# Kernel optimization log

Measured on AMD Instinct MI355X. Metric: run time of the kernel, lower is better.

The kernel has to match this reference:

```python
import jax, jax.numpy as jnp
import numpy as np

EMBED_DIM = 1024
NUM_HEADS = 16
HEAD_DIM = EMBED_DIM // NUM_HEADS  # 64
B, NQ, NK = 4, 1024, 2048


def setup_inputs() -> dict:
    key = jax.random.key(0)
    ks = jax.random.split(key, 13)
    s = 1.0 / np.sqrt(EMBED_DIM)
    inp = {
        "query": jax.random.normal(ks[0], (B, NQ, EMBED_DIM), jnp.float32),
        "key": jax.random.normal(ks[1], (B, NK, EMBED_DIM), jnp.float32),
        "value": jax.random.normal(ks[2], (B, NK, EMBED_DIM), jnp.float32),
        # positive multiplicity weights per key element
        "key_multiplicities": jax.random.uniform(ks[3], (B, NK), jnp.float32, 0.1, 4.0),
        "wq_w": jax.random.normal(ks[4], (EMBED_DIM, EMBED_DIM), jnp.float32) * s,
        "wq_b": jnp.zeros((EMBED_DIM,), jnp.float32),
        "wk_w": jax.random.normal(ks[5], (EMBED_DIM, EMBED_DIM), jnp.float32) * s,
        "wk_b": jnp.zeros((EMBED_DIM,), jnp.float32),
        "wv_w": jax.random.normal(ks[6], (EMBED_DIM, EMBED_DIM), jnp.float32) * s,
        "wv_b": jnp.zeros((EMBED_DIM,), jnp.float32),
        "wo_w": jax.random.normal(ks[7], (EMBED_DIM, EMBED_DIM), jnp.float32) * s,
        "wo_b": jnp.zeros((EMBED_DIM,), jnp.float32),
    }
    return inp


def _split_heads(x, b, n):
    # (b, n, h*d) -> (b, h, n, d)
    return x.reshape(b, n, NUM_HEADS, HEAD_DIM).transpose(0, 2, 1, 3)


def reference(query, key, value, key_multiplicities,
              wq_w, wq_b, wk_w, wk_b, wv_w, wv_b, wo_w, wo_b):
    b, n_q, _ = query.shape
    _, n_k, _ = key.shape
    q = _split_heads(query @ wq_w.T + wq_b, b, n_q)   # (b, h, n_q, d)
    k = _split_heads(key @ wk_w.T + wk_b, b, n_k)     # (b, h, n_k, d)
    v = _split_heads(value @ wv_w.T + wv_b, b, n_k)   # (b, h, n_k, d)
    scale = 1.0 / jnp.sqrt(jnp.asarray(HEAD_DIM, q.dtype))
    scores = jnp.einsum("bhqd,bhkd->bhqk", q, k) * scale
    # multiplicities weight each key: softmax_i(m_i * exp(s_i)) == softmax(s_i + log m_i)
    logits = scores + jnp.log(key_multiplicities)[:, None, None, :]
    attn = jax.nn.softmax(logits, axis=-1)            # (b, h, n_q, n_k)
    out = jnp.einsum("bhqk,bhkd->bhqd", attn, v)
    out = out.transpose(0, 2, 1, 3).reshape(b, n_q, NUM_HEADS * HEAD_DIM)
    return out @ wo_w.T + wo_b
```

## Files before the change

kernel.cpp:

```cpp
#include <hip/hip_runtime.h>
#include <hip/hip_bf16.h>
#include <stdint.h>
#include <stddef.h>

typedef __attribute__((ext_vector_type(8))) short bf16x8;
typedef __attribute__((ext_vector_type(4))) short short4v;
typedef __attribute__((ext_vector_type(4))) float f32x4;
typedef __attribute__((ext_vector_type(2))) uint32_t u32x2;
typedef __attribute__((ext_vector_type(4))) uint32_t u32x4;

#define MFMA16(a, b, c) __builtin_amdgcn_mfma_f32_16x16x32_bf16((a), (b), (c), 0, 0, 0)

__device__ __forceinline__ short f2bf(float f) {
    uint32_t u = __builtin_bit_cast(uint32_t, f);
    u = (u + 0x7FFFu + ((u >> 16) & 1u)) >> 16;
    return (short)(uint16_t)u;
}

__device__ __forceinline__ uint32_t pkbf(float a, float b) {
#if __has_builtin(__builtin_amdgcn_cvt_pk_bf16_f32)
    auto r = __builtin_amdgcn_cvt_pk_bf16_f32(a, b);
    return __builtin_bit_cast(uint32_t, r);
#else
    return (uint32_t)(uint16_t)f2bf(a) | ((uint32_t)(uint16_t)f2bf(b) << 16);
#endif
}

__device__ __forceinline__ float fexp2(float x) {
#if __has_builtin(__builtin_amdgcn_exp2f)
    return __builtin_amdgcn_exp2f(x);
#else
    return exp2f(x);
#endif
}

__device__ __forceinline__ void gload16(const short* g, short* l) {
    __builtin_amdgcn_global_load_lds(
        (const __attribute__((address_space(1))) unsigned int*)g,
        (__attribute__((address_space(3))) unsigned int*)l, 16, 0, 0);
}

__global__ __launch_bounds__(256) void prep_kernel(
        const float* __restrict__ w0, const float* __restrict__ w1,
        const float* __restrict__ w2, const float* __restrict__ w3,
        const float* __restrict__ q, const float* __restrict__ k,
        const float* __restrict__ v, const float* __restrict__ m,
        short* __restrict__ wb, short* __restrict__ Qa,
        short* __restrict__ Ka, short* __restrict__ Va,
        float* __restrict__ lm) {
    const int z = blockIdx.z, bx = blockIdx.x;
    if (z == 7) {
        if (bx >= 4) return;
        const int i = (bx * 256 + threadIdx.x) * 8;
        f32x4 a = *(const f32x4*)(m + i);
        f32x4 b = *(const f32x4*)(m + i + 4);
        f32x4 oa, ob;
        #pragma unroll
        for (int j = 0; j < 4; ++j) { oa[j] = __log2f(a[j]); ob[j] = __log2f(b[j]); }
        *(f32x4*)(lm + i) = oa;
        *(f32x4*)(lm + i + 4) = ob;
        return;
    }
    const float* src;
    short* dst;
    int nb;
    if (z < 4) {
        src = (z == 0) ? w0 : (z == 1) ? w1 : (z == 2) ? w2 : w3;
        dst = wb + (size_t)z * 1048576;
        nb = 512;
    } else if (z == 4) { src = q; dst = Qa; nb = 2048; }
    else if (z == 5)   { src = k; dst = Ka; nb = 4096; }
    else               { src = v; dst = Va; nb = 4096; }
    if (bx >= nb) return;
    const size_t i = ((size_t)bx * 256 + threadIdx.x) * 8;
    f32x4 a = *(const f32x4*)(src + i);
    f32x4 b = *(const f32x4*)(src + i + 4);
    u32x4 o = { pkbf(a[0], a[1]), pkbf(a[2], a[3]), pkbf(b[0], b[1]), pkbf(b[2], b[3]) };
    *(u32x4*)(dst + i) = o;
}


__global__ __launch_bounds__(256) void gemm_qk_kernel(
        const short* __restrict__ Qa, const short* __restrict__ Ka,
        const short* __restrict__ wb, const float* __restrict__ wq_b,
        const float* __restrict__ wk_b, short* __restrict__ Qp,
        short* __restrict__ Kp) {
    __shared__ short As[128 * 32];
    __shared__ short Bs[128 * 32];

    const int y = blockIdx.y;
    const short* A; const short* W; const float* bias; short* out; int nshift, tm;
    if (y < 32) { A = Qa; W = wb;           bias = wq_b; out = Qp; nshift = 10; tm = y * 128; }
    else        { A = Ka; W = wb + 1048576; bias = wk_b; out = Kp; nshift = 11; tm = (y - 32) * 128; }

    const int t = threadIdx.x, lane = t & 63, w = t >> 6;
    const int wr = w >> 1, wc = w & 1;
    const int qd = lane >> 4, c = lane & 15;
    const int tn = blockIdx.x * 128;

    f32x4 acc[4][4];
    #pragma unroll
    for (int i = 0; i < 4; ++i)
        #pragma unroll
        for (int j = 0; j < 4; ++j) acc[i][j] = (f32x4){0.f, 0.f, 0.f, 0.f};

    const int r0 = w * 16 + (lane >> 2);
    const int qc = (lane & 3) ^ ((lane >> 3) & 3);
    const short* ga0 = A + (size_t)(tm + r0) * 1024 + qc * 8;
    const short* ga1 = ga0 + 64 * 1024;
    const short* gb0 = W + (size_t)(tn + r0) * 1024 + qc * 8;
    const short* gb1 = gb0 + 64 * 1024;
    short* la0 = &As[w * 512];
    short* la1 = &As[w * 512 + 2048];
    short* lb0 = &Bs[w * 512];
    short* lb1 = &Bs[w * 512 + 2048];
    const int swz = (qd ^ ((c >> 1) & 3)) * 8;

    for (int k0 = 0; k0 < 1024; k0 += 32) {
        __syncthreads();
        gload16(ga0 + k0, la0);
        gload16(ga1 + k0, la1);
        gload16(gb0 + k0, lb0);
        gload16(gb1 + k0, lb1);
        __syncthreads();
        bf16x8 af[4], bfr[4];
        #pragma unroll
        for (int rt = 0; rt < 4; ++rt)
            af[rt] = *(const bf16x8*)&As[(wr * 64 + rt * 16 + c) * 32 + swz];
        #pragma unroll
        for (int ct = 0; ct < 4; ++ct)
            bfr[ct] = *(const bf16x8*)&Bs[(wc * 64 + ct * 16 + c) * 32 + swz];
        #pragma unroll
        for (int rt = 0; rt < 4; ++rt)
            #pragma unroll
            for (int ct = 0; ct < 4; ++ct)
                acc[rt][ct] = MFMA16(af[rt], bfr[ct], acc[rt][ct]);
    }

    float bv[4];
    #pragma unroll
    for (int ct = 0; ct < 4; ++ct) bv[ct] = bias[tn + wc * 64 + ct * 16 + c];

    const int mask = (1 << nshift) - 1;
    #pragma unroll
    for (int rt = 0; rt < 4; ++rt)
        #pragma unroll
        for (int ct = 0; ct < 4; ++ct) {
            const int cg = tn + wc * 64 + ct * 16 + c;
            const int h = cg >> 6, d = cg & 63;
            #pragma unroll
            for (int r = 0; r < 4; ++r) {
                const int rg = tm + wr * 64 + rt * 16 + qd * 4 + r;
                const int bb = rg >> nshift, n = rg & mask;
                out[((((size_t)(bb * 16 + h)) << nshift) + n) * 64 + d] =
                    f2bf(acc[rt][ct][r] + bv[ct]);
            }
        }
}

__global__ __launch_bounds__(256) void gemm_v_kernel(
        const short* __restrict__ Va, const short* __restrict__ W,
        const float* __restrict__ bias, short* __restrict__ Vt) {
    __shared__ short As[128 * 32];
    __shared__ short Bs[128 * 32];

    const int t = threadIdx.x, lane = t & 63, w = t >> 6;
    const int wr = w >> 1, wc = w & 1;
    const int qd = lane >> 4, c = lane & 15;
    const int tm = blockIdx.y * 128, tn = blockIdx.x * 128;

    f32x4 acc[4][4];
    #pragma unroll
    for (int i = 0; i < 4; ++i)
        #pragma unroll
        for (int j = 0; j < 4; ++j) acc[i][j] = (f32x4){0.f, 0.f, 0.f, 0.f};

    const int r0 = w * 16 + (lane >> 2);
    const int qc = (lane & 3) ^ ((lane >> 3) & 3);
    const short* ga0 = Va + (size_t)(tm + r0) * 1024 + qc * 8;
    const short* ga1 = ga0 + 64 * 1024;
    const short* gb0 = W + (size_t)(tn + r0) * 1024 + qc * 8;
    const short* gb1 = gb0 + 64 * 1024;
    short* la0 = &As[w * 512];
    short* la1 = &As[w * 512 + 2048];
    short* lb0 = &Bs[w * 512];
    short* lb1 = &Bs[w * 512 + 2048];
    const int swz = (qd ^ ((c >> 1) & 3)) * 8;

    for (int k0 = 0; k0 < 1024; k0 += 32) {
        __syncthreads();
        gload16(ga0 + k0, la0);
        gload16(ga1 + k0, la1);
        gload16(gb0 + k0, lb0);
        gload16(gb1 + k0, lb1);
        __syncthreads();
        bf16x8 af[4], bfr[4];
        #pragma unroll
        for (int rt = 0; rt < 4; ++rt)
            af[rt] = *(const bf16x8*)&As[(wr * 64 + rt * 16 + c) * 32 + swz];
        #pragma unroll
        for (int ct = 0; ct < 4; ++ct)
            bfr[ct] = *(const bf16x8*)&Bs[(wc * 64 + ct * 16 + c) * 32 + swz];
        #pragma unroll
        for (int rt = 0; rt < 4; ++rt)
            #pragma unroll
            for (int ct = 0; ct < 4; ++ct)
                acc[rt][ct] = MFMA16(af[rt], bfr[ct], acc[rt][ct]);
    }

    float bv[4];
    #pragma unroll
    for (int ct = 0; ct < 4; ++ct) bv[ct] = bias[tn + wc * 64 + ct * 16 + c];

    #pragma unroll
    for (int rt = 0; rt < 4; ++rt)
        #pragma unroll
        for (int ct = 0; ct < 4; ++ct) {
            const int cg = tn + wc * 64 + ct * 16 + c;
            const int h = cg >> 6, d = cg & 63;
            const int rg0 = tm + wr * 64 + rt * 16 + qd * 4;
            const int bb = rg0 >> 11, n = rg0 & 2047;
            u32x2 pk = { pkbf(acc[rt][ct][0] + bv[ct], acc[rt][ct][1] + bv[ct]),
                         pkbf(acc[rt][ct][2] + bv[ct], acc[rt][ct][3] + bv[ct]) };
            *(u32x2*)&Vt[((((size_t)(bb * 16 + h)) * 64 + d) << 11) + n] = pk;
        }
}

__global__ __launch_bounds__(256) void gemm_o_kernel(
        const short* __restrict__ Ob, const short* __restrict__ W,
        const float* __restrict__ bias, float* __restrict__ out) {
    __shared__ short As[128 * 32];
    __shared__ short Bs[64 * 32];

    const int t = threadIdx.x, lane = t & 63, w = t >> 6;
    const int wr = w >> 1, wc = w & 1;
    const int qd = lane >> 4, c = lane & 15;
    const int tm = blockIdx.y * 128, tn = blockIdx.x * 64;

    f32x4 acc[4][2];
    #pragma unroll
    for (int i = 0; i < 4; ++i)
        #pragma unroll
        for (int j = 0; j < 2; ++j) acc[i][j] = (f32x4){0.f, 0.f, 0.f, 0.f};

    const int r0 = w * 16 + (lane >> 2);
    const int qc = (lane & 3) ^ ((lane >> 3) & 3);
    const short* ga0 = Ob + (size_t)(tm + r0) * 1024 + qc * 8;
    const short* ga1 = ga0 + 64 * 1024;
    const short* gb0 = W + (size_t)(tn + r0) * 1024 + qc * 8;
    short* la0 = &As[w * 512];
    short* la1 = &As[w * 512 + 2048];
    short* lb0 = &Bs[w * 512];
    const int swz = (qd ^ ((c >> 1) & 3)) * 8;

    for (int k0 = 0; k0 < 1024; k0 += 32) {
        __syncthreads();
        gload16(ga0 + k0, la0);
        gload16(ga1 + k0, la1);
        gload16(gb0 + k0, lb0);
        __syncthreads();
        bf16x8 af[4], bfr[2];
        #pragma unroll
        for (int rt = 0; rt < 4; ++rt)
            af[rt] = *(const bf16x8*)&As[(wr * 64 + rt * 16 + c) * 32 + swz];
        #pragma unroll
        for (int ct = 0; ct < 2; ++ct)
            bfr[ct] = *(const bf16x8*)&Bs[(wc * 32 + ct * 16 + c) * 32 + swz];
        #pragma unroll
        for (int rt = 0; rt < 4; ++rt)
            #pragma unroll
            for (int ct = 0; ct < 2; ++ct)
                acc[rt][ct] = MFMA16(af[rt], bfr[ct], acc[rt][ct]);
    }

    float bv[2];
    #pragma unroll
    for (int ct = 0; ct < 2; ++ct) bv[ct] = bias[tn + wc * 32 + ct * 16 + c];

    #pragma unroll
    for (int rt = 0; rt < 4; ++rt)
        #pragma unroll
        for (int ct = 0; ct < 2; ++ct) {
            const int cg = tn + wc * 32 + ct * 16 + c;
            #pragma unroll
            for (int r = 0; r < 4; ++r) {
                const int rg = tm + wr * 64 + rt * 16 + qd * 4 + r;
                out[(size_t)rg * 1024 + cg] = acc[rt][ct][r] + bv[ct];
            }
        }
}

__global__ __launch_bounds__(256, 2) void attn_kernel(
        const short* __restrict__ Qp, const short* __restrict__ Kp,
        const short* __restrict__ Vt, const float* __restrict__ logm,
        short* __restrict__ Ob) {
    __shared__ short UKP[128 * 136];
    __shared__ short Vs[64 * 136];
    __shared__ float Lm[128];
    short* Ks = UKP;
    short* Ps = UKP;

    const int qt = blockIdx.x, bh = blockIdx.y;
    const int b = bh >> 4;
    const int t = threadIdx.x, lane = t & 63, w = t >> 6;
    const int qd = lane >> 4, c = lane & 15;
    const float SC = 0.18033688011112042f;

    bf16x8 qf[2][2];
    #pragma unroll
    for (int ct = 0; ct < 2; ++ct)
        #pragma unroll
        for (int kd = 0; kd < 2; ++kd)
            qf[ct][kd] = *(const bf16x8*)(Qp +
                ((size_t)bh * 1024 + qt * 128 + w * 32 + ct * 16 + c) * 64 + kd * 32 + qd * 8);

    float mo[2] = {-1e30f, -1e30f};
    float li[2] = {0.f, 0.f};
    f32x4 oacc[2][4];
    #pragma unroll
    for (int i = 0; i < 2; ++i)
        #pragma unroll
        for (int j = 0; j < 4; ++j) oacc[i][j] = (f32x4){0.f, 0.f, 0.f, 0.f};

    const short* kg = Kp + ((size_t)bh * 2048 + (t >> 1)) * 64 + (t & 1) * 32;
    const short* vg = Vt + ((size_t)bh * 64 + (t >> 2)) * 2048 + (t & 3) * 32;

    for (int kt = 0; kt < 16; ++kt) {
        const short* kp = kg + (size_t)kt * 128 * 64;
        bf16x8 kx0 = *(const bf16x8*)(kp);
        bf16x8 kx1 = *(const bf16x8*)(kp + 8);
        bf16x8 kx2 = *(const bf16x8*)(kp + 16);
        bf16x8 kx3 = *(const bf16x8*)(kp + 24);
        const short* vp = vg + kt * 128;
        bf16x8 vx0 = *(const bf16x8*)(vp);
        bf16x8 vx1 = *(const bf16x8*)(vp + 8);
        bf16x8 vx2 = *(const bf16x8*)(vp + 16);
        bf16x8 vx3 = *(const bf16x8*)(vp + 24);
        float lmv = 0.f;
        if (t < 128) lmv = logm[b * 2048 + kt * 128 + t];

        {
            const int kr = t >> 1, kc = (t & 1) * 32;
            *(bf16x8*)&Ks[kr * 72 + kc]      = kx0;
            *(bf16x8*)&Ks[kr * 72 + kc + 8]  = kx1;
            *(bf16x8*)&Ks[kr * 72 + kc + 16] = kx2;
            *(bf16x8*)&Ks[kr * 72 + kc + 24] = kx3;
            const int vr = t >> 2, vc = (t & 3) * 32;
            *(bf16x8*)&Vs[vr * 136 + vc]      = vx0;
            *(bf16x8*)&Vs[vr * 136 + vc + 8]  = vx1;
            *(bf16x8*)&Vs[vr * 136 + vc + 16] = vx2;
            *(bf16x8*)&Vs[vr * 136 + vc + 24] = vx3;
            if (t < 128) Lm[t] = lmv;
        }
        __syncthreads();

        f32x4 s[8][2];
        #pragma unroll
        for (int rt = 0; rt < 8; ++rt) {
            bf16x8 a0 = *(const bf16x8*)&Ks[(rt * 16 + c) * 72 + qd * 8];
            bf16x8 a1 = *(const bf16x8*)&Ks[(rt * 16 + c) * 72 + 32 + qd * 8];
            #pragma unroll
            for (int ct = 0; ct < 2; ++ct) {
                f32x4 z = (f32x4){0.f, 0.f, 0.f, 0.f};
                f32x4 p0 = MFMA16(a0, qf[ct][0], z);
                s[rt][ct] = MFMA16(a1, qf[ct][1], p0);
            }
        }
        __syncthreads();

        float mt[2] = {-1e30f, -1e30f};
        #pragma unroll
        for (int rt = 0; rt < 8; ++rt) {
            f32x4 lv = *(const f32x4*)&Lm[rt * 16 + qd * 4];
            #pragma unroll
            for (int ct = 0; ct < 2; ++ct)
                #pragma unroll
                for (int r = 0; r < 4; ++r) {
                    float vv = s[rt][ct][r] * SC + lv[r];
                    s[rt][ct][r] = vv;
                    mt[ct] = fmaxf(mt[ct], vv);
                }
        }
        float al[2], snew[2];
        #pragma unroll
        for (int ct = 0; ct < 2; ++ct) {
            mt[ct] = fmaxf(mt[ct], __shfl_xor(mt[ct], 16));
            mt[ct] = fmaxf(mt[ct], __shfl_xor(mt[ct], 32));
            float mn = fmaxf(mo[ct], mt[ct]);
            al[ct] = fexp2(mo[ct] - mn);
            mo[ct] = mn;
            snew[ct] = 0.f;
        }
        #pragma unroll
        for (int rt = 0; rt < 8; ++rt) {
            #pragma unroll
            for (int ct = 0; ct < 2; ++ct) {
                float p0 = fexp2(s[rt][ct][0] - mo[ct]);
                float p1 = fexp2(s[rt][ct][1] - mo[ct]);
                float p2 = fexp2(s[rt][ct][2] - mo[ct]);
                float p3 = fexp2(s[rt][ct][3] - mo[ct]);
                snew[ct] += (p0 + p1) + (p2 + p3);
                u32x2 pk = { pkbf(p0, p1), pkbf(p2, p3) };
                *(u32x2*)&Ps[(w * 32 + ct * 16 + c) * 136 + rt * 16 + qd * 4] = pk;
            }
        }
        #pragma unroll
        for (int ct = 0; ct < 2; ++ct) {
            snew[ct] += __shfl_xor(snew[ct], 16);
            snew[ct] += __shfl_xor(snew[ct], 32);
            li[ct] = li[ct] * al[ct] + snew[ct];
        }

        float alr[2][4];
        #pragma unroll
        for (int rtq = 0; rtq < 2; ++rtq)
            #pragma unroll
            for (int r = 0; r < 4; ++r)
                alr[rtq][r] = __shfl(al[rtq], qd * 4 + r);
        #pragma unroll
        for (int rtq = 0; rtq < 2; ++rtq)
            #pragma unroll
            for (int ct = 0; ct < 4; ++ct)
                #pragma unroll
                for (int r = 0; r < 4; ++r)
                    oacc[rtq][ct][r] *= alr[rtq][r];

        #pragma unroll
        for (int kk = 0; kk < 4; ++kk) {
            bf16x8 pf[2], vf[4];
            #pragma unroll
            for (int rtq = 0; rtq < 2; ++rtq)
                pf[rtq] = *(const bf16x8*)&Ps[(w * 32 + rtq * 16 + c) * 136 + kk * 32 + qd * 8];
            #pragma unroll
            for (int ct = 0; ct < 4; ++ct)
                vf[ct] = *(const bf16x8*)&Vs[(ct * 16 + c) * 136 + kk * 32 + qd * 8];
            #pragma unroll
            for (int rtq = 0; rtq < 2; ++rtq)
                #pragma unroll
                for (int ct = 0; ct < 4; ++ct)
                    oacc[rtq][ct] = MFMA16(pf[rtq], vf[ct], oacc[rtq][ct]);
        }
        __syncthreads();
    }

    const int h = bh & 15;
    float inv[2][4];
    #pragma unroll
    for (int rtq = 0; rtq < 2; ++rtq)
        #pragma unroll
        for (int r = 0; r < 4; ++r)
            inv[rtq][r] = 1.f / __shfl(li[rtq], qd * 4 + r);
    #pragma unroll
    for (int rtq = 0; rtq < 2; ++rtq)
        #pragma unroll
        for (int ct = 0; ct < 4; ++ct)
            #pragma unroll
            for (int r = 0; r < 4; ++r) {
                const int qg = qt * 128 + w * 32 + rtq * 16 + qd * 4 + r;
                const int e = h * 64 + ct * 16 + c;
                Ob[((size_t)(b * 1024 + qg)) * 1024 + e] = f2bf(oacc[rtq][ct][r] * inv[rtq][r]);
            }
}

extern "C" void kernel_launch(void* const* d_in, const int* in_sizes, int n_in,
                              void* d_out, int out_size, void* d_ws, size_t ws_size,
                              hipStream_t stream) {
    (void)in_sizes; (void)n_in; (void)out_size; (void)ws_size;
    const float* query = (const float*)d_in[0];
    const float* key   = (const float*)d_in[1];
    const float* value = (const float*)d_in[2];
    const float* mult  = (const float*)d_in[3];
    const float* wq_w  = (const float*)d_in[4];
    const float* wq_b  = (const float*)d_in[5];
    const float* wk_w  = (const float*)d_in[6];
    const float* wk_b  = (const float*)d_in[7];
    const float* wv_w  = (const float*)d_in[8];
    const float* wv_b  = (const float*)d_in[9];
    const float* wo_w  = (const float*)d_in[10];
    const float* wo_b  = (const float*)d_in[11];
    float* out = (float*)d_out;

    char* ws = (char*)d_ws;
    const size_t MB = 1024 * 1024;
    short* wb = (short*)(ws + 0 * MB);
    short* Qa = (short*)(ws + 8 * MB);
    short* Ka = (short*)(ws + 16 * MB);
    short* Va = (short*)(ws + 32 * MB);
    short* Vt = (short*)(ws + 8 * MB);
    short* Ob = (short*)(ws + 32 * MB);
    short* Qp = (short*)(ws + 48 * MB);
    short* Kp = (short*)(ws + 56 * MB);
    float* lm = (float*)(ws + 72 * MB);

    prep_kernel<<<dim3(4096, 1, 8), 256, 0, stream>>>(
        wq_w, wk_w, wv_w, wo_w, query, key, value, mult, wb, Qa, Ka, Va, lm);
    gemm_qk_kernel<<<dim3(8, 96), 256, 0, stream>>>(Qa, Ka, wb, wq_b, wk_b, Qp, Kp);
    gemm_v_kernel<<<dim3(8, 64), 256, 0, stream>>>(Va, wb + 2097152, wv_b, Vt);
    attn_kernel<<<dim3(8, 64), 256, 0, stream>>>(Qp, Kp, Vt, lm, Ob);
    gemm_o_kernel<<<dim3(16, 32), 256, 0, stream>>>(Ob, wb + 3145728, wo_b, out);
}
```

Before: 297.4 us.

## Merge Q/K/V projections into one launch and halve attention query tile

```diff
diff --git a/kernel.cpp b/kernel.cpp
--- a/kernel.cpp
+++ b/kernel.cpp
@@ -79,19 +79,20 @@
     *(u32x4*)(dst + i) = o;
 }
 
-
-__global__ __launch_bounds__(256) void gemm_qk_kernel(
+__global__ __launch_bounds__(256) void proj_kernel(
         const short* __restrict__ Qa, const short* __restrict__ Ka,
-        const short* __restrict__ wb, const float* __restrict__ wq_b,
-        const float* __restrict__ wk_b, short* __restrict__ Qp,
-        short* __restrict__ Kp) {
+        const short* __restrict__ Va, const short* __restrict__ wb,
+        const float* __restrict__ wq_b, const float* __restrict__ wk_b,
+        const float* __restrict__ wv_b, short* __restrict__ Qp,
+        short* __restrict__ Kp, short* __restrict__ Vt, const int ybase) {
     __shared__ short As[128 * 32];
     __shared__ short Bs[128 * 32];
 
-    const int y = blockIdx.y;
-    const short* A; const short* W; const float* bias; short* out; int nshift, tm;
-    if (y < 32) { A = Qa; W = wb;           bias = wq_b; out = Qp; nshift = 10; tm = y * 128; }
-    else        { A = Ka; W = wb + 1048576; bias = wk_b; out = Kp; nshift = 11; tm = (y - 32) * 128; }
+    const int y = blockIdx.y + ybase;
+    const short* A; const short* W; const float* bias; int mode, tm;
+    if (y < 32)      { A = Qa; W = wb;           bias = wq_b; mode = 0; tm = y * 128; }
+    else if (y < 96) { A = Ka; W = wb + 1048576; bias = wk_b; mode = 1; tm = (y - 32) * 128; }
+    else             { A = Va; W = wb + 2097152; bias = wv_b; mode = 2; tm = (y - 96) * 128; }
 
     const int t = threadIdx.x, lane = t & 63, w = t >> 6;
     const int wr = w >> 1, wc = w & 1;
@@ -141,89 +142,38 @@
     #pragma unroll
     for (int ct = 0; ct < 4; ++ct) bv[ct] = bias[tn + wc * 64 + ct * 16 + c];
 
-    const int mask = (1 << nshift) - 1;
-    #pragma unroll
-    for (int rt = 0; rt < 4; ++rt)
-        #pragma unroll
-        for (int ct = 0; ct < 4; ++ct) {
-            const int cg = tn + wc * 64 + ct * 16 + c;
-            const int h = cg >> 6, d = cg & 63;
-            #pragma unroll
-            for (int r = 0; r < 4; ++r) {
-                const int rg = tm + wr * 64 + rt * 16 + qd * 4 + r;
-                const int bb = rg >> nshift, n = rg & mask;
-                out[((((size_t)(bb * 16 + h)) << nshift) + n) * 64 + d] =
-                    f2bf(acc[rt][ct][r] + bv[ct]);
+    if (mode == 2) {
+        #pragma unroll
+        for (int rt = 0; rt < 4; ++rt)
+            #pragma unroll
+            for (int ct = 0; ct < 4; ++ct) {
+                const int cg = tn + wc * 64 + ct * 16 + c;
+                const int h = cg >> 6, d = cg & 63;
+                const int rg0 = tm + wr * 64 + rt * 16 + qd * 4;
+                const int bb = rg0 >> 11, n = rg0 & 2047;
+                u32x2 pk = { pkbf(acc[rt][ct][0] + bv[ct], acc[rt][ct][1] + bv[ct]),
+                             pkbf(acc[rt][ct][2] + bv[ct], acc[rt][ct][3] + bv[ct]) };
+                *(u32x2*)&Vt[((((size_t)(bb * 16 + h)) * 64 + d) << 11) + n] = pk;
             }
-        }
-}
-
-__global__ __launch_bounds__(256) void gemm_v_kernel(
-        const short* __restrict__ Va, const short* __restrict__ W,
-        const float* __restrict__ bias, short* __restrict__ Vt) {
-    __shared__ short As[128 * 32];
-    __shared__ short Bs[128 * 32];
-
-    const int t = threadIdx.x, lane = t & 63, w = t >> 6;
-    const int wr = w >> 1, wc = w & 1;
-    const int qd = lane >> 4, c = lane & 15;
-    const int tm = blockIdx.y * 128, tn = blockIdx.x * 128;
-
-    f32x4 acc[4][4];
-    #pragma unroll
-    for (int i = 0; i < 4; ++i)
-        #pragma unroll
-        for (int j = 0; j < 4; ++j) acc[i][j] = (f32x4){0.f, 0.f, 0.f, 0.f};
-
-    const int r0 = w * 16 + (lane >> 2);
-    const int qc = (lane & 3) ^ ((lane >> 3) & 3);
-    const short* ga0 = Va + (size_t)(tm + r0) * 1024 + qc * 8;
-    const short* ga1 = ga0 + 64 * 1024;
-    const short* gb0 = W + (size_t)(tn + r0) * 1024 + qc * 8;
-    const short* gb1 = gb0 + 64 * 1024;
-    short* la0 = &As[w * 512];
-    short* la1 = &As[w * 512 + 2048];
-    short* lb0 = &Bs[w * 512];
-    short* lb1 = &Bs[w * 512 + 2048];
-    const int swz = (qd ^ ((c >> 1) & 3)) * 8;
-
-    for (int k0 = 0; k0 < 1024; k0 += 32) {
-        __syncthreads();
-        gload16(ga0 + k0, la0);
-        gload16(ga1 + k0, la1);
-        gload16(gb0 + k0, lb0);
-        gload16(gb1 + k0, lb1);
-        __syncthreads();
-        bf16x8 af[4], bfr[4];
-        #pragma unroll
-        for (int rt = 0; rt < 4; ++rt)
-            af[rt] = *(const bf16x8*)&As[(wr * 64 + rt * 16 + c) * 32 + swz];
-        #pragma unroll
-        for (int ct = 0; ct < 4; ++ct)
-            bfr[ct] = *(const bf16x8*)&Bs[(wc * 64 + ct * 16 + c) * 32 + swz];
-        #pragma unroll
-        for (int rt = 0; rt < 4; ++rt)
-            #pragma unroll
-            for (int ct = 0; ct < 4; ++ct)
-                acc[rt][ct] = MFMA16(af[rt], bfr[ct], acc[rt][ct]);
-    }
-
-    float bv[4];
-    #pragma unroll
-    for (int ct = 0; ct < 4; ++ct) bv[ct] = bias[tn + wc * 64 + ct * 16 + c];
-
-    #pragma unroll
-    for (int rt = 0; rt < 4; ++rt)
-        #pragma unroll
-        for (int ct = 0; ct < 4; ++ct) {
-            const int cg = tn + wc * 64 + ct * 16 + c;
-            const int h = cg >> 6, d = cg & 63;
-            const int rg0 = tm + wr * 64 + rt * 16 + qd * 4;
-            const int bb = rg0 >> 11, n = rg0 & 2047;
-            u32x2 pk = { pkbf(acc[rt][ct][0] + bv[ct], acc[rt][ct][1] + bv[ct]),
-                         pkbf(acc[rt][ct][2] + bv[ct], acc[rt][ct][3] + bv[ct]) };
-            *(u32x2*)&Vt[((((size_t)(bb * 16 + h)) * 64 + d) << 11) + n] = pk;
-        }
+    } else {
+        short* out = (mode == 0) ? Qp : Kp;
+        const int nshift = (mode == 0) ? 10 : 11;
+        const int mask = (1 << nshift) - 1;
+        #pragma unroll
+        for (int rt = 0; rt < 4; ++rt)
+            #pragma unroll
+            for (int ct = 0; ct < 4; ++ct) {
+                const int cg = tn + wc * 64 + ct * 16 + c;
+                const int h = cg >> 6, d = cg & 63;
+                #pragma unroll
+                for (int r = 0; r < 4; ++r) {
+                    const int rg = tm + wr * 64 + rt * 16 + qd * 4 + r;
+                    const int bb = rg >> nshift, n = rg & mask;
+                    out[((((size_t)(bb * 16 + h)) << nshift) + n) * 64 + d] =
+                        f2bf(acc[rt][ct][r] + bv[ct]);
+                }
+            }
+    }
 }
 
 __global__ __launch_bounds__(256) void gemm_o_kernel(
@@ -290,11 +240,11 @@
         }
 }
 
-__global__ __launch_bounds__(256, 2) void attn_kernel(
+__global__ __launch_bounds__(256, 4) void attn_kernel(
         const short* __restrict__ Qp, const short* __restrict__ Kp,
         const short* __restrict__ Vt, const float* __restrict__ logm,
         short* __restrict__ Ob) {
-    __shared__ short UKP[128 * 136];
+    __shared__ short UKP[9216];
     __shared__ short Vs[64 * 136];
     __shared__ float Lm[128];
     short* Ks = UKP;
@@ -306,21 +256,16 @@
     const int qd = lane >> 4, c = lane & 15;
     const float SC = 0.18033688011112042f;
 
-    bf16x8 qf[2][2];
-    #pragma unroll
-    for (int ct = 0; ct < 2; ++ct)
-        #pragma unroll
-        for (int kd = 0; kd < 2; ++kd)
-            qf[ct][kd] = *(const bf16x8*)(Qp +
-                ((size_t)bh * 1024 + qt * 128 + w * 32 + ct * 16 + c) * 64 + kd * 32 + qd * 8);
-
-    float mo[2] = {-1e30f, -1e30f};
-    float li[2] = {0.f, 0.f};
-    f32x4 oacc[2][4];
-    #pragma unroll
-    for (int i = 0; i < 2; ++i)
-        #pragma unroll
-        for (int j = 0; j < 4; ++j) oacc[i][j] = (f32x4){0.f, 0.f, 0.f, 0.f};
+    bf16x8 qf[2];
+    #pragma unroll
+    for (int kd = 0; kd < 2; ++kd)
+        qf[kd] = *(const bf16x8*)(Qp +
+            ((size_t)bh * 1024 + qt * 64 + w * 16 + c) * 64 + kd * 32 + qd * 8);
+
+    float mo = -1e30f, li = 0.f;
+    f32x4 oacc[4];
+    #pragma unroll
+    for (int j = 0; j < 4; ++j) oacc[j] = (f32x4){0.f, 0.f, 0.f, 0.f};
 
     const short* kg = Kp + ((size_t)bh * 2048 + (t >> 1)) * 64 + (t & 1) * 32;
     const short* vg = Vt + ((size_t)bh * 64 + (t >> 2)) * 2048 + (t & 3) * 32;
@@ -354,118 +299,88 @@
         }
         __syncthreads();
 
-        f32x4 s[8][2];
+        f32x4 s[8];
         #pragma unroll
         for (int rt = 0; rt < 8; ++rt) {
             bf16x8 a0 = *(const bf16x8*)&Ks[(rt * 16 + c) * 72 + qd * 8];
             bf16x8 a1 = *(const bf16x8*)&Ks[(rt * 16 + c) * 72 + 32 + qd * 8];
-            #pragma unroll
-            for (int ct = 0; ct < 2; ++ct) {
-                f32x4 z = (f32x4){0.f, 0.f, 0.f, 0.f};
-                f32x4 p0 = MFMA16(a0, qf[ct][0], z);
-                s[rt][ct] = MFMA16(a1, qf[ct][1], p0);
-            }
-        }
-        __syncthreads();
-
-        float mt[2] = {-1e30f, -1e30f};
+            f32x4 z = (f32x4){0.f, 0.f, 0.f, 0.f};
+            s[rt] = MFMA16(a1, qf[1], MFMA16(a0, qf[0], z));
+        }
+        __syncthreads();
+
+        float mt = -1e30f;
         #pragma unroll
         for (int rt = 0; rt < 8; ++rt) {
             f32x4 lv = *(const f32x4*)&Lm[rt * 16 + qd * 4];
             #pragma unroll
-            for (int ct = 0; ct < 2; ++ct)
-                #pragma unroll
-                for (int r = 0; r < 4; ++r) {
-                    float vv = s[rt][ct][r] * SC + lv[r];
-                    s[rt][ct][r] = vv;
-                    mt[ct] = fmaxf(mt[ct], vv);
-                }
-        }
-        float al[2], snew[2];
-        #pragma unroll
-        for (int ct = 0; ct < 2; ++ct) {
-            mt[ct] = fmaxf(mt[ct], __shfl_xor(mt[ct], 16));
-            mt[ct] = fmaxf(mt[ct], __shfl_xor(mt[ct], 32));
-            float mn = fmaxf(mo[ct], mt[ct]);
-            al[ct] = fexp2(mo[ct] - mn);
-            mo[ct] = mn;
-            snew[ct] = 0.f;
-        }
+            for (int r = 0; r < 4; ++r) {
+                float vv = s[rt][r] * SC + lv[r];
+                s[rt][r] = vv;
+                mt = fmaxf(mt, vv);
+            }
+        }
+        mt = fmaxf(mt, __shfl_xor(mt, 16));
+        mt = fmaxf(mt, __shfl_xor(mt, 32));
+        const float mn = fmaxf(mo, mt);
+        const float al = fexp2(mo - mn);
+        mo = mn;
+        float snew = 0.f;
         #pragma unroll
         for (int rt = 0; rt < 8; ++rt) {
-            #pragma unroll
-            for (int ct = 0; ct < 2; ++ct) {
-                float p0 = fexp2(s[rt][ct][0] - mo[ct]);
-                float p1 = fexp2(s[rt][ct][1] - mo[ct]);
-                float p2 = fexp2(s[rt][ct][2] - mo[ct]);
-                float p3 = fexp2(s[rt][ct][3] - mo[ct]);
-                snew[ct] += (p0 + p1) + (p2 + p3);
-                u32x2 pk = { pkbf(p0, p1), pkbf(p2, p3) };
-                *(u32x2*)&Ps[(w * 32 + ct * 16 + c) * 136 + rt * 16 + qd * 4] = pk;
-            }
-        }
-        #pragma unroll
-        for (int ct = 0; ct < 2; ++ct) {
-            snew[ct] += __shfl_xor(snew[ct], 16);
-            snew[ct] += __shfl_xor(snew[ct], 32);
-            li[ct] = li[ct] * al[ct] + snew[ct];
-        }
-
-        float alr[2][4];
-        #pragma unroll
-        for (int rtq = 0; rtq < 2; ++rtq)
+            float p0 = fexp2(s[rt][0] - mo);
+            float p1 = fexp2(s[rt][1] - mo);
+            float p2 = fexp2(s[rt][2] - mo);
+            float p3 = fexp2(s[rt][3] - mo);
+            snew += (p0 + p1) + (p2 + p3);
+            u32x2 pk = { pkbf(p0, p1), pkbf(p2, p3) };
+            *(u32x2*)&Ps[(w * 16 + c) * 136 + rt * 16 + qd * 4] = pk;
+        }
+        snew += __shfl_xor(snew, 16);
+        snew += __shfl_xor(snew, 32);
+        li = li * al + snew;
+
+        float alr[4];
+        #pragma unroll
+        for (int r = 0; r < 4; ++r) alr[r] = __shfl(al, qd * 4 + r);
+        #pragma unroll
+        for (int ct = 0; ct < 4; ++ct)
             #pragma unroll
             for (int r = 0; r < 4; ++r)
-                alr[rtq][r] = __shfl(al[rtq], qd * 4 + r);
-        #pragma unroll
-        for (int rtq = 0; rtq < 2; ++rtq)
-            #pragma unroll
-            for (int ct = 0; ct < 4; ++ct)
-                #pragma unroll
-                for (int r = 0; r < 4; ++r)
-                    oacc[rtq][ct][r] *= alr[rtq][r];
+                oacc[ct][r] *= alr[r];
 
         #pragma unroll
         for (int kk = 0; kk < 4; ++kk) {
-            bf16x8 pf[2], vf[4];
-            #pragma unroll
-            for (int rtq = 0; rtq < 2; ++rtq)
-                pf[rtq] = *(const bf16x8*)&Ps[(w * 32 + rtq * 16 + c) * 136 + kk * 32 + qd * 8];
+            bf16x8 pf = *(const bf16x8*)&Ps[(w * 16 + c) * 136 + kk * 32 + qd * 8];
+            bf16x8 vf[4];
             #pragma unroll
             for (int ct = 0; ct < 4; ++ct)
                 vf[ct] = *(const bf16x8*)&Vs[(ct * 16 + c) * 136 + kk * 32 + qd * 8];
             #pragma unroll
-            for (int rtq = 0; rtq < 2; ++rtq)
-                #pragma unroll
-                for (int ct = 0; ct < 4; ++ct)
-                    oacc[rtq][ct] = MFMA16(pf[rtq], vf[ct], oacc[rtq][ct]);
+            for (int ct = 0; ct < 4; ++ct)
+                oacc[ct] = MFMA16(pf, vf[ct], oacc[ct]);
         }
         __syncthreads();
     }
 
     const int h = bh & 15;
-    float inv[2][4];
-    #pragma unroll
-    for (int rtq = 0; rtq < 2; ++rtq)
-        #pragma unroll
-        for (int r = 0; r < 4; ++r)
-            inv[rtq][r] = 1.f / __shfl(li[rtq], qd * 4 + r);
-    #pragma unroll
-    for (int rtq = 0; rtq < 2; ++rtq)
-        #pragma unroll
-        for (int ct = 0; ct < 4; ++ct)
-            #pragma unroll
-            for (int r = 0; r < 4; ++r) {
-                const int qg = qt * 128 + w * 32 + rtq * 16 + qd * 4 + r;
-                const int e = h * 64 + ct * 16 + c;
-                Ob[((size_t)(b * 1024 + qg)) * 1024 + e] = f2bf(oacc[rtq][ct][r] * inv[rtq][r]);
-            }
+    float inv[4];
+    #pragma unroll
+    for (int r = 0; r < 4; ++r) inv[r] = 1.f / __shfl(li, qd * 4 + r);
+    #pragma unroll
+    for (int ct = 0; ct < 4; ++ct)
+        #pragma unroll
+        for (int r = 0; r < 4; ++r) {
+            const int qg = qt * 64 + w * 16 + qd * 4 + r;
+            const int e = h * 64 + ct * 16 + c;
+            Ob[((size_t)(b * 1024 + qg)) * 1024 + e] = f2bf(oacc[ct][r] * inv[r]);
+        }
 }
 
 extern "C" void kernel_launch(void* const* d_in, const int* in_sizes, int n_in,
                               void* d_out, int out_size, void* d_ws, size_t ws_size,
                               hipStream_t stream) {
-    (void)in_sizes; (void)n_in; (void)out_size; (void)ws_size;
+    (void)in_sizes; (void)n_in; (void)out_size;
     const float* query = (const float*)d_in[0];
     const float* key   = (const float*)d_in[1];
     const float* value = (const float*)d_in[2];
@@ -482,20 +397,36 @@
 
     char* ws = (char*)d_ws;
     const size_t MB = 1024 * 1024;
+    const bool merged = ws_size >= 89 * MB;
+
     short* wb = (short*)(ws + 0 * MB);
     short* Qa = (short*)(ws + 8 * MB);
     short* Ka = (short*)(ws + 16 * MB);
     short* Va = (short*)(ws + 32 * MB);
-    short* Vt = (short*)(ws + 8 * MB);
-    short* Ob = (short*)(ws + 32 * MB);
     short* Qp = (short*)(ws + 48 * MB);
     short* Kp = (short*)(ws + 56 * MB);
-    float* lm = (float*)(ws + 72 * MB);
+    short *Vt, *Ob; float* lm;
+    if (merged) {
+        Vt = (short*)(ws + 72 * MB);
+        Ob = (short*)(ws + 8 * MB);
+        lm = (float*)(ws + 88 * MB);
+    } else {
+        Vt = (short*)(ws + 8 * MB);
+        Ob = (short*)(ws + 32 * MB);
+        lm = (float*)(ws + 72 * MB);
+    }
 
     prep_kernel<<<dim3(4096, 1, 8), 256, 0, stream>>>(
         wq_w, wk_w, wv_w, wo_w, query, key, value, mult, wb, Qa, Ka, Va, lm);
-    gemm_qk_kernel<<<dim3(8, 96), 256, 0, stream>>>(Qa, Ka, wb, wq_b, wk_b, Qp, Kp);
-    gemm_v_kernel<<<dim3(8, 64), 256, 0, stream>>>(Va, wb + 2097152, wv_b, Vt);
-    attn_kernel<<<dim3(8, 64), 256, 0, stream>>>(Qp, Kp, Vt, lm, Ob);
+    if (merged) {
+        proj_kernel<<<dim3(8, 160), 256, 0, stream>>>(
+            Qa, Ka, Va, wb, wq_b, wk_b, wv_b, Qp, Kp, Vt, 0);
+    } else {
+        proj_kernel<<<dim3(8, 96), 256, 0, stream>>>(
+            Qa, Ka, Va, wb, wq_b, wk_b, wv_b, Qp, Kp, Vt, 0);
+        proj_kernel<<<dim3(8, 64), 256, 0, stream>>>(
+            Qa, Ka, Va, wb, wq_b, wk_b, wv_b, Qp, Kp, Vt, 96);
+    }
+    attn_kernel<<<dim3(16, 64), 256, 0, stream>>>(Qp, Kp, Vt, lm, Ob);
     gemm_o_kernel<<<dim3(16, 32), 256, 0, stream>>>(Ob, wb + 3145728, wo_b, out);
 }
```

Result: slower. 318.6 us (+7.1%).

## Merge QKV projections, async-load K/V in attention with XOR swizzle, remap blocks per XCD

Applied to the files above, without the earlier changes.

```diff
diff --git a/kernel.cpp b/kernel.cpp
--- a/kernel.cpp
+++ b/kernel.cpp
@@ -79,19 +79,20 @@
     *(u32x4*)(dst + i) = o;
 }
 
-
-__global__ __launch_bounds__(256) void gemm_qk_kernel(
+__global__ __launch_bounds__(256, 3) void proj_kernel(
         const short* __restrict__ Qa, const short* __restrict__ Ka,
-        const short* __restrict__ wb, const float* __restrict__ wq_b,
-        const float* __restrict__ wk_b, short* __restrict__ Qp,
-        short* __restrict__ Kp) {
+        const short* __restrict__ Va, const short* __restrict__ wb,
+        const float* __restrict__ wq_b, const float* __restrict__ wk_b,
+        const float* __restrict__ wv_b, short* __restrict__ Qp,
+        short* __restrict__ Kp, short* __restrict__ Vt, const int ybase) {
     __shared__ short As[128 * 32];
     __shared__ short Bs[128 * 32];
 
-    const int y = blockIdx.y;
-    const short* A; const short* W; const float* bias; short* out; int nshift, tm;
-    if (y < 32) { A = Qa; W = wb;           bias = wq_b; out = Qp; nshift = 10; tm = y * 128; }
-    else        { A = Ka; W = wb + 1048576; bias = wk_b; out = Kp; nshift = 11; tm = (y - 32) * 128; }
+    const int y = blockIdx.y + ybase;
+    const short* A; const short* W; const float* bias; int mode, tm;
+    if (y < 32)      { A = Qa; W = wb;           bias = wq_b; mode = 0; tm = y * 128; }
+    else if (y < 96) { A = Ka; W = wb + 1048576; bias = wk_b; mode = 1; tm = (y - 32) * 128; }
+    else             { A = Va; W = wb + 2097152; bias = wv_b; mode = 2; tm = (y - 96) * 128; }
 
     const int t = threadIdx.x, lane = t & 63, w = t >> 6;
     const int wr = w >> 1, wc = w & 1;
@@ -141,92 +142,41 @@
     #pragma unroll
     for (int ct = 0; ct < 4; ++ct) bv[ct] = bias[tn + wc * 64 + ct * 16 + c];
 
-    const int mask = (1 << nshift) - 1;
-    #pragma unroll
-    for (int rt = 0; rt < 4; ++rt)
-        #pragma unroll
-        for (int ct = 0; ct < 4; ++ct) {
-            const int cg = tn + wc * 64 + ct * 16 + c;
-            const int h = cg >> 6, d = cg & 63;
-            #pragma unroll
-            for (int r = 0; r < 4; ++r) {
-                const int rg = tm + wr * 64 + rt * 16 + qd * 4 + r;
-                const int bb = rg >> nshift, n = rg & mask;
-                out[((((size_t)(bb * 16 + h)) << nshift) + n) * 64 + d] =
-                    f2bf(acc[rt][ct][r] + bv[ct]);
-            }
-        }
-}
-
-__global__ __launch_bounds__(256) void gemm_v_kernel(
-        const short* __restrict__ Va, const short* __restrict__ W,
-        const float* __restrict__ bias, short* __restrict__ Vt) {
-    __shared__ short As[128 * 32];
-    __shared__ short Bs[128 * 32];
-
-    const int t = threadIdx.x, lane = t & 63, w = t >> 6;
-    const int wr = w >> 1, wc = w & 1;
-    const int qd = lane >> 4, c = lane & 15;
-    const int tm = blockIdx.y * 128, tn = blockIdx.x * 128;
-
-    f32x4 acc[4][4];
-    #pragma unroll
-    for (int i = 0; i < 4; ++i)
-        #pragma unroll
-        for (int j = 0; j < 4; ++j) acc[i][j] = (f32x4){0.f, 0.f, 0.f, 0.f};
-
-    const int r0 = w * 16 + (lane >> 2);
-    const int qc = (lane & 3) ^ ((lane >> 3) & 3);
-    const short* ga0 = Va + (size_t)(tm + r0) * 1024 + qc * 8;
-    const short* ga1 = ga0 + 64 * 1024;
-    const short* gb0 = W + (size_t)(tn + r0) * 1024 + qc * 8;
-    const short* gb1 = gb0 + 64 * 1024;
-    short* la0 = &As[w * 512];
-    short* la1 = &As[w * 512 + 2048];
-    short* lb0 = &Bs[w * 512];
-    short* lb1 = &Bs[w * 512 + 2048];
-    const int swz = (qd ^ ((c >> 1) & 3)) * 8;
-
-    for (int k0 = 0; k0 < 1024; k0 += 32) {
-        __syncthreads();
-        gload16(ga0 + k0, la0);
-        gload16(ga1 + k0, la1);
-        gload16(gb0 + k0, lb0);
-        gload16(gb1 + k0, lb1);
-        __syncthreads();
-        bf16x8 af[4], bfr[4];
-        #pragma unroll
-        for (int rt = 0; rt < 4; ++rt)
-            af[rt] = *(const bf16x8*)&As[(wr * 64 + rt * 16 + c) * 32 + swz];
-        #pragma unroll
-        for (int ct = 0; ct < 4; ++ct)
-            bfr[ct] = *(const bf16x8*)&Bs[(wc * 64 + ct * 16 + c) * 32 + swz];
-        #pragma unroll
-        for (int rt = 0; rt < 4; ++rt)
-            #pragma unroll
-            for (int ct = 0; ct < 4; ++ct)
-                acc[rt][ct] = MFMA16(af[rt], bfr[ct], acc[rt][ct]);
-    }
-
-    float bv[4];
-    #pragma unroll
-    for (int ct = 0; ct < 4; ++ct) bv[ct] = bias[tn + wc * 64 + ct * 16 + c];
-
-    #pragma unroll
-    for (int rt = 0; rt < 4; ++rt)
-        #pragma unroll
-        for (int ct = 0; ct < 4; ++ct) {
-            const int cg = tn + wc * 64 + ct * 16 + c;
-            const int h = cg >> 6, d = cg & 63;
-            const int rg0 = tm + wr * 64 + rt * 16 + qd * 4;
-            const int bb = rg0 >> 11, n = rg0 & 2047;
-            u32x2 pk = { pkbf(acc[rt][ct][0] + bv[ct], acc[rt][ct][1] + bv[ct]),
-                         pkbf(acc[rt][ct][2] + bv[ct], acc[rt][ct][3] + bv[ct]) };
-            *(u32x2*)&Vt[((((size_t)(bb * 16 + h)) * 64 + d) << 11) + n] = pk;
-        }
-}
-
-__global__ __launch_bounds__(256) void gemm_o_kernel(
+    if (mode == 2) {
+        #pragma unroll
+        for (int rt = 0; rt < 4; ++rt)
+            #pragma unroll
+            for (int ct = 0; ct < 4; ++ct) {
+                const int cg = tn + wc * 64 + ct * 16 + c;
+                const int h = cg >> 6, d = cg & 63;
+                const int rg0 = tm + wr * 64 + rt * 16 + qd * 4;
+                const int bb = rg0 >> 11, n = rg0 & 2047;
+                u32x2 pk = { pkbf(acc[rt][ct][0] + bv[ct], acc[rt][ct][1] + bv[ct]),
+                             pkbf(acc[rt][ct][2] + bv[ct], acc[rt][ct][3] + bv[ct]) };
+                *(u32x2*)&Vt[((((size_t)(bb * 16 + h)) * 64 + d) << 11) + n] = pk;
+            }
+    } else {
+        short* out = (mode == 0) ? Qp : Kp;
+        const int nshift = (mode == 0) ? 10 : 11;
+        const int mask = (1 << nshift) - 1;
+        #pragma unroll
+        for (int rt = 0; rt < 4; ++rt)
+            #pragma unroll
+            for (int ct = 0; ct < 4; ++ct) {
+                const int cg = tn + wc * 64 + ct * 16 + c;
+                const int h = cg >> 6, d = cg & 63;
+                #pragma unroll
+                for (int r = 0; r < 4; ++r) {
+                    const int rg = tm + wr * 64 + rt * 16 + qd * 4 + r;
+                    const int bb = rg >> nshift, n = rg & mask;
+                    out[((((size_t)(bb * 16 + h)) << nshift) + n) * 64 + d] =
+                        f2bf(acc[rt][ct][r] + bv[ct]);
+                }
+            }
+    }
+}
+
+__global__ __launch_bounds__(256, 4) void gemm_o_kernel(
         const short* __restrict__ Ob, const short* __restrict__ W,
         const float* __restrict__ bias, float* __restrict__ out) {
     __shared__ short As[128 * 32];
@@ -294,16 +244,18 @@
         const short* __restrict__ Qp, const short* __restrict__ Kp,
         const short* __restrict__ Vt, const float* __restrict__ logm,
         short* __restrict__ Ob) {
-    __shared__ short UKP[128 * 136];
-    __shared__ short Vs[64 * 136];
+    __shared__ short Ps[128 * 128];
+    __shared__ short Vs[64 * 128];
     __shared__ float Lm[128];
-    short* Ks = UKP;
-    short* Ps = UKP;
-
-    const int qt = blockIdx.x, bh = blockIdx.y;
+    short* Ks = Ps;
+
+    const int bid = blockIdx.x;
+    const int xcd = bid & 7, ii = bid >> 3;
+    const int qt = ii >> 3, bh = xcd + ((ii & 7) << 3);
     const int b = bh >> 4;
     const int t = threadIdx.x, lane = t & 63, w = t >> 6;
     const int qd = lane >> 4, c = lane & 15;
+    const int cl = c & 7;
     const float SC = 0.18033688011112042f;
 
     bf16x8 qf[2][2];
@@ -322,48 +274,44 @@
         #pragma unroll
         for (int j = 0; j < 4; ++j) oacc[i][j] = (f32x4){0.f, 0.f, 0.f, 0.f};
 
-    const short* kg = Kp + ((size_t)bh * 2048 + (t >> 1)) * 64 + (t & 1) * 32;
-    const short* vg = Vt + ((size_t)bh * 64 + (t >> 2)) * 2048 + (t & 3) * 32;
+    const short* kgp[4];
+    short* klp[4];
+    const short* vgp[4];
+    short* vlp[4];
+    {
+        const int krow = lane >> 3;
+        const int kchk = (lane & 7) ^ krow;
+        const int vrow = lane >> 4;
+        #pragma unroll
+        for (int i = 0; i < 4; ++i) {
+            const int rk = w * 32 + i * 8 + krow;
+            kgp[i] = Kp + ((size_t)bh * 2048 + rk) * 64 + kchk * 8;
+            klp[i] = &Ks[(w * 4 + i) * 512];
+            const int rv = w * 16 + i * 4 + vrow;
+            const int vchk = (lane & 15) ^ (rv & 7);
+            vgp[i] = Vt + ((size_t)bh * 64 + rv) * 2048 + vchk * 8;
+            vlp[i] = &Vs[(w * 4 + i) * 512];
+        }
+    }
 
     for (int kt = 0; kt < 16; ++kt) {
-        const short* kp = kg + (size_t)kt * 128 * 64;
-        bf16x8 kx0 = *(const bf16x8*)(kp);
-        bf16x8 kx1 = *(const bf16x8*)(kp + 8);
-        bf16x8 kx2 = *(const bf16x8*)(kp + 16);
-        bf16x8 kx3 = *(const bf16x8*)(kp + 24);
-        const short* vp = vg + kt * 128;
-        bf16x8 vx0 = *(const bf16x8*)(vp);
-        bf16x8 vx1 = *(const bf16x8*)(vp + 8);
-        bf16x8 vx2 = *(const bf16x8*)(vp + 16);
-        bf16x8 vx3 = *(const bf16x8*)(vp + 24);
-        float lmv = 0.f;
-        if (t < 128) lmv = logm[b * 2048 + kt * 128 + t];
-
-        {
-            const int kr = t >> 1, kc = (t & 1) * 32;
-            *(bf16x8*)&Ks[kr * 72 + kc]      = kx0;
-            *(bf16x8*)&Ks[kr * 72 + kc + 8]  = kx1;
-            *(bf16x8*)&Ks[kr * 72 + kc + 16] = kx2;
-            *(bf16x8*)&Ks[kr * 72 + kc + 24] = kx3;
-            const int vr = t >> 2, vc = (t & 3) * 32;
-            *(bf16x8*)&Vs[vr * 136 + vc]      = vx0;
-            *(bf16x8*)&Vs[vr * 136 + vc + 8]  = vx1;
-            *(bf16x8*)&Vs[vr * 136 + vc + 16] = vx2;
-            *(bf16x8*)&Vs[vr * 136 + vc + 24] = vx3;
-            if (t < 128) Lm[t] = lmv;
-        }
+        #pragma unroll
+        for (int i = 0; i < 4; ++i) {
+            gload16(kgp[i] + (size_t)kt * 8192, klp[i]);
+            gload16(vgp[i] + kt * 128, vlp[i]);
+        }
+        if (t < 128) Lm[t] = logm[b * 2048 + kt * 128 + t];
         __syncthreads();
 
         f32x4 s[8][2];
         #pragma unroll
         for (int rt = 0; rt < 8; ++rt) {
-            bf16x8 a0 = *(const bf16x8*)&Ks[(rt * 16 + c) * 72 + qd * 8];
-            bf16x8 a1 = *(const bf16x8*)&Ks[(rt * 16 + c) * 72 + 32 + qd * 8];
+            bf16x8 a0 = *(const bf16x8*)&Ks[(rt * 16 + c) * 64 + (qd ^ cl) * 8];
+            bf16x8 a1 = *(const bf16x8*)&Ks[(rt * 16 + c) * 64 + ((4 | qd) ^ cl) * 8];
             #pragma unroll
             for (int ct = 0; ct < 2; ++ct) {
                 f32x4 z = (f32x4){0.f, 0.f, 0.f, 0.f};
-                f32x4 p0 = MFMA16(a0, qf[ct][0], z);
-                s[rt][ct] = MFMA16(a1, qf[ct][1], p0);
+                s[rt][ct] = MFMA16(a1, qf[ct][1], MFMA16(a0, qf[ct][0], z));
             }
         }
         __syncthreads();
@@ -401,7 +349,9 @@
                 float p3 = fexp2(s[rt][ct][3] - mo[ct]);
                 snew[ct] += (p0 + p1) + (p2 + p3);
                 u32x2 pk = { pkbf(p0, p1), pkbf(p2, p3) };
-                *(u32x2*)&Ps[(w * 32 + ct * 16 + c) * 136 + rt * 16 + qd * 4] = pk;
+                const int prow = w * 32 + ct * 16 + c;
+                const int pch = (2 * rt + (qd >> 1)) ^ cl;
+                *(u32x2*)&Ps[prow * 128 + pch * 8 + (qd & 1) * 4] = pk;
             }
         }
         #pragma unroll
@@ -427,13 +377,14 @@
 
         #pragma unroll
         for (int kk = 0; kk < 4; ++kk) {
+            const int lch = ((kk * 4 + qd) ^ cl) * 8;
             bf16x8 pf[2], vf[4];
             #pragma unroll
             for (int rtq = 0; rtq < 2; ++rtq)
-                pf[rtq] = *(const bf16x8*)&Ps[(w * 32 + rtq * 16 + c) * 136 + kk * 32 + qd * 8];
+                pf[rtq] = *(const bf16x8*)&Ps[(w * 32 + rtq * 16 + c) * 128 + lch];
             #pragma unroll
             for (int ct = 0; ct < 4; ++ct)
-                vf[ct] = *(const bf16x8*)&Vs[(ct * 16 + c) * 136 + kk * 32 + qd * 8];
+                vf[ct] = *(const bf16x8*)&Vs[(ct * 16 + c) * 128 + lch];
             #pragma unroll
             for (int rtq = 0; rtq < 2; ++rtq)
                 #pragma unroll
@@ -465,7 +416,7 @@
 extern "C" void kernel_launch(void* const* d_in, const int* in_sizes, int n_in,
                               void* d_out, int out_size, void* d_ws, size_t ws_size,
                               hipStream_t stream) {
-    (void)in_sizes; (void)n_in; (void)out_size; (void)ws_size;
+    (void)in_sizes; (void)n_in; (void)out_size;
     const float* query = (const float*)d_in[0];
     const float* key   = (const float*)d_in[1];
     const float* value = (const float*)d_in[2];
@@ -482,20 +433,36 @@
 
     char* ws = (char*)d_ws;
     const size_t MB = 1024 * 1024;
+    const bool merged = ws_size >= 89 * MB;
+
     short* wb = (short*)(ws + 0 * MB);
     short* Qa = (short*)(ws + 8 * MB);
     short* Ka = (short*)(ws + 16 * MB);
     short* Va = (short*)(ws + 32 * MB);
-    short* Vt = (short*)(ws + 8 * MB);
-    short* Ob = (short*)(ws + 32 * MB);
     short* Qp = (short*)(ws + 48 * MB);
     short* Kp = (short*)(ws + 56 * MB);
-    float* lm = (float*)(ws + 72 * MB);
+    short *Vt, *Ob; float* lm;
+    if (merged) {
+        Vt = (short*)(ws + 72 * MB);
+        Ob = (short*)(ws + 8 * MB);
+        lm = (float*)(ws + 88 * MB);
+    } else {
+        Vt = (short*)(ws + 8 * MB);
+        Ob = (short*)(ws + 32 * MB);
+        lm = (float*)(ws + 72 * MB);
+    }
 
     prep_kernel<<<dim3(4096, 1, 8), 256, 0, stream>>>(
         wq_w, wk_w, wv_w, wo_w, query, key, value, mult, wb, Qa, Ka, Va, lm);
-    gemm_qk_kernel<<<dim3(8, 96), 256, 0, stream>>>(Qa, Ka, wb, wq_b, wk_b, Qp, Kp);
-    gemm_v_kernel<<<dim3(8, 64), 256, 0, stream>>>(Va, wb + 2097152, wv_b, Vt);
-    attn_kernel<<<dim3(8, 64), 256, 0, stream>>>(Qp, Kp, Vt, lm, Ob);
+    if (merged) {
+        proj_kernel<<<dim3(8, 160), 256, 0, stream>>>(
+            Qa, Ka, Va, wb, wq_b, wk_b, wv_b, Qp, Kp, Vt, 0);
+    } else {
+        proj_kernel<<<dim3(8, 96), 256, 0, stream>>>(
+            Qa, Ka, Va, wb, wq_b, wk_b, wv_b, Qp, Kp, Vt, 0);
+        proj_kernel<<<dim3(8, 64), 256, 0, stream>>>(
+            Qa, Ka, Va, wb, wq_b, wk_b, wv_b, Qp, Kp, Vt, 96);
+    }
+    attn_kernel<<<dim3(512), 256, 0, stream>>>(Qp, Kp, Vt, lm, Ob);
     gemm_o_kernel<<<dim3(16, 32), 256, 0, stream>>>(Ob, wb + 3145728, wo_b, out);
 }
```

After: 297.4 us. About the same (-0.0%).
